# Optimization experiments

Measured on AMD Instinct MI355X. Metric: run time of the kernel, lower is better.

The kernel has to match this reference:

```python
import jax, jax.numpy as jnp
import numpy as np

H, C = 2, 32  # heads, out_channels per head
NEG_SLOPE = 0.2


def gatv2_layer(h, src, dst, ea, W, b, We, att, bias, N):
    # shared lin_l = lin_r (share_weights=True)
    z = (h @ W + b).reshape(N, H, C)                      # [N,H,C]
    e = (ea @ We).reshape(-1, H, C)                        # [E',H,C]
    s = jax.nn.leaky_relu(z[dst] + z[src] + e, NEG_SLOPE)  # [E',H,C]
    alpha = jnp.einsum('ehc,hc->eh', s, att)               # [E',H]
    # segment softmax over destination neighborhoods
    m = jax.ops.segment_max(alpha, dst, num_segments=N)
    m = jnp.where(jnp.isfinite(m), m, 0.0)
    ex = jnp.exp(alpha - m[dst])
    denom = jax.ops.segment_sum(ex, dst, num_segments=N)
    a = ex / (denom[dst] + 1e-16)                          # [E',H]
    msg = (z[src] * a[:, :, None]).reshape(-1, H * C)      # [E',H*C]
    out = jax.ops.segment_sum(msg, dst, num_segments=N) + bias
    return out                                             # [N,H*C]


def setup_inputs() -> dict:
    key = jax.random.key(0)
    ks = jax.random.split(key, 16)
    N, E = 50000, 800000
    inp = {
        'x': jax.random.normal(ks[0], (N, 2), jnp.float32),
        'edge_index': jax.random.randint(ks[1], (2, E), 0, N, jnp.int64 if jax.config.jax_enable_x64 else jnp.int32).astype(jnp.int32),
        'edge_attr': jax.random.uniform(ks[2], (E, 2), jnp.float32),
        'dest_index': 123,
        'W0': jax.random.normal(ks[3], (2, 64), jnp.float32) * 0.5,
        'b0': jnp.zeros((64,), jnp.float32),
        'We0': jax.random.normal(ks[4], (2, 64), jnp.float32) * 0.5,
        'att0': jax.random.normal(ks[5], (H, C), jnp.float32) * 0.5,
        'bias0': jnp.zeros((64,), jnp.float32),
        'W1': jax.random.normal(ks[6], (64, 64), jnp.float32) * 0.125,
        'b1': jnp.zeros((64,), jnp.float32),
        'We1': jax.random.normal(ks[7], (2, 64), jnp.float32) * 0.5,
        'att1': jax.random.normal(ks[8], (H, C), jnp.float32) * 0.5,
        'bias1': jnp.zeros((64,), jnp.float32),
        'Wm1': jax.random.normal(ks[9], (194, 32), jnp.float32) * 0.07,
        'bm1': jnp.zeros((32,), jnp.float32),
        'Wm2': jax.random.normal(ks[10], (32, 1), jnp.float32) * 0.17,
        'bm2': jnp.zeros((1,), jnp.float32),
    }
    return inp


def reference(x, edge_index, edge_attr, dest_index,
              W0, b0, We0, att0, bias0,
              W1, b1, We1, att1, bias1,
              Wm1, bm1, Wm2, bm2):
    N = x.shape[0]
    # add self loops (fill_value='mean' for edge_attr)
    loops = jnp.arange(N, dtype=edge_index.dtype)
    src = jnp.concatenate([edge_index[0], loops])
    dst = jnp.concatenate([edge_index[1], loops])
    ea_sl = jnp.concatenate(
        [edge_attr, jnp.broadcast_to(edge_attr.mean(axis=0), (N, edge_attr.shape[1]))], axis=0)

    h = x
    h = jax.nn.elu(gatv2_layer(h, src, dst, ea_sl, W0, b0, We0, att0, bias0, N))
    h = jax.nn.elu(gatv2_layer(h, src, dst, ea_sl, W1, b1, We1, att1, bias1, N))

    goal = h[dest_index]                                   # [64]
    src_emb = h[edge_index[0]]                             # [E,64]
    dst_emb = h[edge_index[1]]                             # [E,64]
    goal_rep = jnp.broadcast_to(goal, (edge_index.shape[1], goal.shape[0]))
    edge_in = jnp.concatenate([src_emb, dst_emb, goal_rep, edge_attr], axis=-1)  # [E,194]
    hmlp = jax.nn.relu(edge_in @ Wm1 + bm1)
    logits = (hmlp @ Wm2 + bm2).squeeze(-1)                # [E]
    return logits
```

## Files before the change

### kernel.cpp

```cpp
#include <hip/hip_runtime.h>
#include <hip/hip_bf16.h>
#include <hip/hip_fp16.h>
#include <math.h>


typedef __attribute__((ext_vector_type(8))) short short8;
typedef __attribute__((ext_vector_type(4))) float f32x4;

#define BSH 7
#define CAP 4096
#define CH 4096

template <int IMM>
__device__ __forceinline__ float swz(float x) {
    return __int_as_float(__builtin_amdgcn_ds_swizzle(__float_as_int(x), IMM));
}

template <int CTRL>
__device__ __forceinline__ float dpp_add(float p) {
    int t = __builtin_amdgcn_update_dpp(0, __float_as_int(p), CTRL, 0xF, 0xF, true);
    return p + __int_as_float(t);
}

__device__ __forceinline__ float head_reduce(float p) {
    p = dpp_add<0xB1>(p);
    p = dpp_add<0x4E>(p);
    p = dpp_add<0x141>(p);
    p = dpp_add<0x140>(p);
    p += swz<0x401F>(p);
    return p;
}

__device__ __forceinline__ short2 bsplit(float x) {
    unsigned u = __float_as_uint(x);
    short hi = (short)(u >> 16);
    float hif = __uint_as_float(u & 0xFFFF0000u);
    short lo = (short)(__float_as_uint(x - hif) >> 16);
    return make_short2(hi, lo);
}

__global__ __launch_bounds__(512) void setup_kernel(const float* __restrict__ W1,
                                                    const float* __restrict__ Wm1,
                                                    short* __restrict__ BfW1,
                                                    short* __restrict__ BfWm,
                                                    int* __restrict__ bucket_cursor,
                                                    float* __restrict__ easum, int nbuck) {
    if (blockIdx.x == 2) {
        for (int i = threadIdx.x; i < nbuck; i += 512) bucket_cursor[i] = i * CAP;
        if (threadIdx.x < 2) easum[threadIdx.x] = 0.f;
        return;
    }
    int snt = threadIdx.x >> 6;
    int lane = threadIdx.x & 63;
    int s = snt >> 2, nt = snt & 3;
    int col = nt * 16 + (lane & 15);
    short* Bf = blockIdx.x == 0 ? BfW1 : BfWm;
#pragma unroll
    for (int j = 0; j < 8; ++j) {
        int k = s * 32 + (lane >> 4) * 8 + j;
        float v;
        if (blockIdx.x == 0) {
            v = W1[k * 64 + col];
        } else {
            v = (col < 32) ? Wm1[k * 32 + col] : Wm1[(64 + k) * 32 + (col - 32)];
        }
        short2 t = bsplit(v);
        Bf[(snt * 2 + 0) * 512 + lane * 8 + j] = t.x;
        Bf[(snt * 2 + 1) * 512 + lane * 8 + j] = t.y;
    }
}

__global__ __launch_bounds__(256) void phaseA_kernel(const int* __restrict__ ei,
                                                     const float2* __restrict__ ea,
                                                     int* __restrict__ bucket_cursor,
                                                     float* __restrict__ easum,
                                                     float4* __restrict__ staged,
                                                     int E, int nbuck) {
    extern __shared__ int sm[];
    int* lcnt = sm;
    int* lbase = sm + nbuck;
    __shared__ float r0[4], r1[4];
    int tid = threadIdx.x;
    for (int i = tid; i < nbuck; i += 256) lcnt[i] = 0;
    __syncthreads();
    int base = blockIdx.x * CH;
    int end = min(base + CH, E);
    for (int i = base + tid; i < end; i += 256) {
        int d = ei[E + i];
        atomicAdd(&lcnt[d >> BSH], 1);
    }
    __syncthreads();
    for (int i = tid; i < nbuck; i += 256) {
        int c = lcnt[i];
        lbase[i] = c ? atomicAdd(&bucket_cursor[i], c) : 0;
        lcnt[i] = 0;
    }
    __syncthreads();
    float s0 = 0.f, s1 = 0.f;
    for (int i = base + tid; i < end; i += 256) {
        int s = ei[i], d = ei[E + i];
        float2 v = ea[i];
        s0 += v.x; s1 += v.y;
        int b = d >> BSH;
        int pos = lbase[b] + atomicAdd(&lcnt[b], 1);
        staged[pos] = make_float4(__int_as_float(s), v.x, v.y, __int_as_float(d));
    }
#pragma unroll
    for (int o = 32; o >= 1; o >>= 1) {
        s0 += __shfl_xor(s0, o);
        s1 += __shfl_xor(s1, o);
    }
    int wave = tid >> 6;
    if ((tid & 63) == 0) { r0[wave] = s0; r1[wave] = s1; }
    __syncthreads();
    if (tid == 0) {
        atomicAdd(&easum[0], r0[0] + r0[1] + r0[2] + r0[3]);
        atomicAdd(&easum[1], r1[0] + r1[1] + r1[2] + r1[3]);
    }
}

__global__ __launch_bounds__(256) void bscan_kernel(const int* __restrict__ bucket_cursor,
                                                    int* __restrict__ bucket_base,
                                                    int* __restrict__ row_ptr,
                                                    int N, int nbuck) {
    __shared__ int sm[256];
    int tid = threadIdx.x;
    int K = (nbuck + 255) / 256;
    int b0 = tid * K;
    int local = 0;
    for (int k = 0; k < K; ++k) {
        int b = b0 + k;
        if (b < nbuck) {
            int nodes = min(128, N - (b << BSH));
            local += bucket_cursor[b] - b * CAP + nodes;
        }
    }
    sm[tid] = local;
    __syncthreads();
    for (int st = 1; st < 256; st <<= 1) {
        int v = sm[tid];
        int a = (tid >= st) ? sm[tid - st] : 0;
        __syncthreads();
        sm[tid] = v + a;
        __syncthreads();
    }
    int run = (tid == 0) ? 0 : sm[tid - 1];
    for (int k = 0; k < K; ++k) {
        int b = b0 + k;
        if (b < nbuck) {
            int nodes = min(128, N - (b << BSH));
            int c = bucket_cursor[b] - b * CAP + nodes;
            bucket_base[b] = run;
            run += c;
        }
    }
    if (tid == 255) {
        bucket_base[nbuck] = sm[255];
        row_ptr[N] = sm[255];
    }
}

__global__ __launch_bounds__(256) void phaseB_kernel(const float4* __restrict__ staged,
                                                     const int* __restrict__ bucket_base,
                                                     const int* __restrict__ bucket_cursor,
                                                     const float* __restrict__ easum,
                                                     int* __restrict__ row_ptr,
                                                     float4* __restrict__ recs,
                                                     int N, int E) {
    __shared__ int cnt128[128];
    __shared__ int offs[128];
    int b = blockIdx.x;
    int n0 = b << BSH;
    int tid = threadIdx.x;
    if (tid < 128) cnt128[tid] = 0;
    __syncthreads();
    int sbeg = b * CAP;
    int send = bucket_cursor[b];
    for (int i = sbeg + tid; i < send; i += 256) {
        int d = __float_as_int(staged[i].w);
        atomicAdd(&cnt128[d - n0], 1);
    }
    __syncthreads();
    int node = n0 + tid;
    int tot = 0;
    if (tid < 128) {
        tot = cnt128[tid] + ((node < N) ? 1 : 0);
        offs[tid] = tot;
    }
    __syncthreads();
    for (int st = 1; st < 128; st <<= 1) {
        int v = 0;
        if (tid < 128) {
            v = offs[tid];
            if (tid >= st) v += offs[tid - st];
        }
        __syncthreads();
        if (tid < 128) offs[tid] = v;
        __syncthreads();
    }
    float inv = 1.f / (float)E;
    float m0 = easum[0] * inv, m1 = easum[1] * inv;
    if (tid < 128 && node < N) {
        int excl = bucket_base[b] + offs[tid] - tot;
        row_ptr[node] = excl;
        recs[excl] = make_float4(__int_as_float(node), m0, m1, __int_as_float(node));
        offs[tid] = excl + 1;
    }
    __syncthreads();
    for (int i = sbeg + tid; i < send; i += 256) {
        float4 r = staged[i];
        int d = __float_as_int(r.w);
        int pos = atomicAdd(&offs[d - n0], 1);
        recs[pos] = r;
    }
}

__global__ __launch_bounds__(256) void wgt0_kernel(const float2* __restrict__ x,
                                                   const float* __restrict__ W0,
                                                   const float* __restrict__ b0,
                                                   const float4* __restrict__ recs,
                                                   const float* __restrict__ We,
                                                   const float* __restrict__ att,
                                                   float4* __restrict__ wrec, int EP) {
    int lane = threadIdx.x & 63;
    int m = lane & 15, quad = lane >> 4;
    int c0 = quad * 8, c1 = 32 + c0;
    float w0a[8], w1a[8], ata[8], w0b[8], w1b[8], atb[8];
    float Wxa[8], Wya[8], bca[8], Wxb[8], Wyb[8], bcb[8];
#pragma unroll
    for (int j = 0; j < 8; ++j) {
        w0a[j] = We[c0 + j];  w1a[j] = We[64 + c0 + j];  ata[j] = att[c0 + j];
        w0b[j] = We[c1 + j];  w1b[j] = We[64 + c1 + j];  atb[j] = att[c1 + j];
        Wxa[j] = W0[c0 + j];  Wya[j] = W0[64 + c0 + j];  bca[j] = b0[c0 + j];
        Wxb[j] = W0[c1 + j];  Wyb[j] = W0[64 + c1 + j];  bcb[j] = b0[c1 + j];
    }
    int ntiles = (EP + 15) >> 4;
    int wid = (blockIdx.x * blockDim.x + threadIdx.x) >> 6;
    int nw = (gridDim.x * blockDim.x) >> 6;
    for (int t = wid; t < ntiles; t += nw) {
        int e = t * 16 + m;
        int ec = e < EP ? e : EP - 1;
        float4 r = recs[ec];
        int s = __float_as_int(r.x);
        int d = __float_as_int(r.w);
        float2 xs = x[s];
        float2 xd = x[d];
        float P0 = 0.f, P1 = 0.f;
#pragma unroll
        for (int j = 0; j < 8; ++j) {
            float zs = fmaf(xs.x, Wxa[j], fmaf(xs.y, Wya[j], bca[j]));
            float zd = fmaf(xd.x, Wxa[j], fmaf(xd.y, Wya[j], bca[j]));
            float t0 = zd + zs + fmaf(r.y, w0a[j], r.z * w1a[j]);
            t0 = fmaxf(t0, 0.2f * t0);
            P0 = fmaf(t0, ata[j], P0);
            float zs1 = fmaf(xs.x, Wxb[j], fmaf(xs.y, Wyb[j], bcb[j]));
            float zd1 = fmaf(xd.x, Wxb[j], fmaf(xd.y, Wyb[j], bcb[j]));
            float t1 = zd1 + zs1 + fmaf(r.y, w0b[j], r.z * w1b[j]);
            t1 = fmaxf(t1, 0.2f * t1);
            P1 = fmaf(t1, atb[j], P1);
        }
        P0 += swz<0x401F>(P0);
        P1 += swz<0x401F>(P1);
        P0 += __shfl_xor(P0, 32);
        P1 += __shfl_xor(P1, 32);
        float w0 = __expf(fminf(P0, 60.f));
        float w1 = __expf(fminf(P1, 60.f));
        if (lane < 16 && e < EP) wrec[e] = make_float4(w0, w1, xs.x, xs.y);
    }
}

__global__ __launch_bounds__(256) void hagg0_kernel(const float4* __restrict__ wrec,
                                                    const int* __restrict__ row_ptr,
                                                    const float* __restrict__ W0,
                                                    const float* __restrict__ b0,
                                                    const float* __restrict__ bias,
                                                    float* __restrict__ hout, int N) {
    int gtid = blockIdx.x * blockDim.x + threadIdx.x;
    int n = gtid >> 6;
    if (n >= N) return;
    n = __builtin_amdgcn_readfirstlane(n);
    int lane = threadIdx.x & 63;
    int beg = row_ptr[n], end = row_ptr[n + 1];
    float a0 = 0.f, a1 = 0.f, a2 = 0.f, c0 = 0.f, c1 = 0.f, c2 = 0.f;
    for (int i = beg + lane; i < end; i += 64) {
        float4 r = wrec[i];
        a0 += r.x; a1 = fmaf(r.x, r.z, a1); a2 = fmaf(r.x, r.w, a2);
        c0 += r.y; c1 = fmaf(r.y, r.z, c1); c2 = fmaf(r.y, r.w, c2);
    }
#pragma unroll
    for (int o = 32; o >= 1; o >>= 1) {
        a0 += __shfl_xor(a0, o); a1 += __shfl_xor(a1, o); a2 += __shfl_xor(a2, o);
        c0 += __shfl_xor(c0, o); c1 += __shfl_xor(c1, o); c2 += __shfl_xor(c2, o);
    }
    int head = lane >> 5;
    float l  = head ? c0 : a0;
    float Sx = head ? c1 : a1;
    float Sy = head ? c2 : a2;
    float num = fmaf(W0[lane], Sx, fmaf(W0[64 + lane], Sy, b0[lane] * l));
    float v = num / (l + 1e-16f) + bias[lane];
    v = (v > 0.f) ? v : expm1f(v);
    hout[(size_t)n * 64 + lane] = v;
}

__global__ __launch_bounds__(256) void agg1_kernel(
    const __half* __restrict__ z, const int* __restrict__ row_ptr,
    const float4* __restrict__ recs,
    const float* __restrict__ We, const float* __restrict__ att,
    const float* __restrict__ bias, float* __restrict__ hout, int N) {
    int gtid = blockIdx.x * blockDim.x + threadIdx.x;
    int n = gtid >> 6;
    if (n >= N) return;
    n = __builtin_amdgcn_readfirstlane(n);
    int lane = threadIdx.x & 63;

    float We0 = We[lane], We1 = We[64 + lane];
    float attj = att[lane];
    float zn = __half2float(z[(size_t)n * 64 + lane]);

    int beg = row_ptr[n], end = row_ptr[n + 1];
    float ll[4] = {0.f, 0.f, 0.f, 0.f};
    float aa[4] = {0.f, 0.f, 0.f, 0.f};
    int i = beg;
    for (; i + 8 <= end; i += 8) {
        float w[8], zs[8];
#pragma unroll
        for (int k = 0; k < 8; ++k) {
            float4 r = recs[i + k];
            int s = __builtin_amdgcn_readfirstlane(__float_as_int(r.x));
            float zv = __half2float(z[(size_t)s * 64 + lane]);
            float sj = zn + zv + fmaf(r.y, We0, r.z * We1);
            sj = fmaxf(sj, 0.2f * sj);
            float alpha = head_reduce(sj * attj);
            w[k] = __expf(fminf(alpha, 60.f));
            zs[k] = zv;
        }
#pragma unroll
        for (int k = 0; k < 8; ++k) {
            ll[k & 3] += w[k];
            aa[k & 3] = fmaf(w[k], zs[k], aa[k & 3]);
        }
    }
    for (; i < end; ++i) {
        float4 r = recs[i];
        int s = __builtin_amdgcn_readfirstlane(__float_as_int(r.x));
        float zv = __half2float(z[(size_t)s * 64 + lane]);
        float sj = zn + zv + fmaf(r.y, We0, r.z * We1);
        sj = fmaxf(sj, 0.2f * sj);
        float alpha = head_reduce(sj * attj);
        float w = __expf(fminf(alpha, 60.f));
        ll[0] += w;
        aa[0] = fmaf(w, zv, aa[0]);
    }
    float l = (ll[0] + ll[1]) + (ll[2] + ll[3]);
    float a = (aa[0] + aa[1]) + (aa[2] + aa[3]);
    float v = a / (l + 1e-16f) + bias[lane];
    v = (v > 0.f) ? v : expm1f(v);
    hout[(size_t)n * 64 + lane] = v;
}

__global__ __launch_bounds__(256) void mfma_gemm64(const float* __restrict__ h,
                                                   const short* __restrict__ Bf,
                                                   const float* __restrict__ bias,
                                                   __half* __restrict__ out, int N,
                                                   const float* __restrict__ Wm1,
                                                   const float* __restrict__ bm1,
                                                   const int* __restrict__ dest,
                                                   float* __restrict__ gv) {
    int wave = threadIdx.x >> 6;
    int lane = threadIdx.x & 63;
    int n0 = blockIdx.x * 64 + wave * 16;
    if (n0 < N) {
        int m = lane & 15, quad = lane >> 4;
        int arow = n0 + m;
        if (arow > N - 1) arow = N - 1;
        f32x4 acc[4] = {{0.f, 0.f, 0.f, 0.f}, {0.f, 0.f, 0.f, 0.f},
                        {0.f, 0.f, 0.f, 0.f}, {0.f, 0.f, 0.f, 0.f}};
#pragma unroll
        for (int s = 0; s < 2; ++s) {
            const float* ap = h + (size_t)arow * 64 + s * 32 + quad * 8;
            float4 a0 = *(const float4*)ap;
            float4 a1 = *(const float4*)(ap + 4);
            short8 ahi, alo;
            short2 t;
            t = bsplit(a0.x); ahi[0] = t.x; alo[0] = t.y;
            t = bsplit(a0.y); ahi[1] = t.x; alo[1] = t.y;
            t = bsplit(a0.z); ahi[2] = t.x; alo[2] = t.y;
            t = bsplit(a0.w); ahi[3] = t.x; alo[3] = t.y;
            t = bsplit(a1.x); ahi[4] = t.x; alo[4] = t.y;
            t = bsplit(a1.y); ahi[5] = t.x; alo[5] = t.y;
            t = bsplit(a1.z); ahi[6] = t.x; alo[6] = t.y;
            t = bsplit(a1.w); ahi[7] = t.x; alo[7] = t.y;
#pragma unroll
            for (int nt = 0; nt < 4; ++nt) {
                const short* bp = Bf + ((s * 4 + nt) * 2) * 512 + lane * 8;
                short8 bhi = *(const short8*)bp;
                short8 blo = *(const short8*)(bp + 512);
                acc[nt] = __builtin_amdgcn_mfma_f32_16x16x32_bf16(ahi, bhi, acc[nt], 0, 0, 0);
                acc[nt] = __builtin_amdgcn_mfma_f32_16x16x32_bf16(ahi, blo, acc[nt], 0, 0, 0);
                acc[nt] = __builtin_amdgcn_mfma_f32_16x16x32_bf16(alo, bhi, acc[nt], 0, 0, 0);
            }
        }
#pragma unroll
        for (int nt = 0; nt < 4; ++nt) {
            int col = nt * 16 + m;
            float bj = bias ? bias[col] : 0.f;
#pragma unroll
            for (int r = 0; r < 4; ++r) {
                int orow = n0 + quad * 4 + r;
                if (orow < N) out[(size_t)orow * 64 + col] = __float2half(acc[nt][r] + bj);
            }
        }
    }
    if (gv && blockIdx.x == 0 && threadIdx.x < 32) {
        int dd = dest[0];
        int q = threadIdx.x;
        float acc2 = bm1[q];
        for (int k = 0; k < 64; ++k)
            acc2 = fmaf(h[(size_t)dd * 64 + k], Wm1[(128 + k) * 32 + q], acc2);
        gv[q] = acc2;
    }
}

__global__ __launch_bounds__(256) void edge_mlp_kernel(
    const int* __restrict__ ei, const float2* __restrict__ ea,
    const __half* __restrict__ hsd, const float* __restrict__ gvec,
    const float* __restrict__ WrowA, const float* __restrict__ WrowB,
    const float* __restrict__ Wm2, const float* __restrict__ bm2,
    float* __restrict__ out, int E) {
    int tid = blockIdx.x * blockDim.x + threadIdx.x;
    int e = tid >> 3;
    int j = tid & 7;
    if (e >= E) return;
    int s = ei[e], d = ei[E + e];
    float2 eav = ea[e];
    const __half2* ps = (const __half2*)(hsd + (size_t)s * 64 + j * 4);
    const __half2* pd = (const __half2*)(hsd + (size_t)d * 64 + 32 + j * 4);
    float2 a01 = __half22float2(ps[0]), a23 = __half22float2(ps[1]);
    float2 b01 = __half22float2(pd[0]), b23 = __half22float2(pd[1]);
    float4 g = *(const float4*)(gvec + j * 4);
    float4 wa = *(const float4*)(WrowA + j * 4);
    float4 wb = *(const float4*)(WrowB + j * 4);
    float4 w2 = *(const float4*)(Wm2 + j * 4);
    float acc = 0.f, v;
    v = fmaf(eav.x, wa.x, fmaf(eav.y, wb.x, a01.x + b01.x + g.x)); v = fmaxf(v, 0.f); acc = fmaf(v, w2.x, acc);
    v = fmaf(eav.x, wa.y, fmaf(eav.y, wb.y, a01.y + b01.y + g.y)); v = fmaxf(v, 0.f); acc = fmaf(v, w2.y, acc);
    v = fmaf(eav.x, wa.z, fmaf(eav.y, wb.z, a23.x + b23.x + g.z)); v = fmaxf(v, 0.f); acc = fmaf(v, w2.z, acc);
    v = fmaf(eav.x, wa.w, fmaf(eav.y, wb.w, a23.y + b23.y + g.w)); v = fmaxf(v, 0.f); acc = fmaf(v, w2.w, acc);
    acc = dpp_add<0xB1>(acc);
    acc = dpp_add<0x4E>(acc);
    acc = dpp_add<0x141>(acc);
    if (j == 0) out[e] = acc + bm2[0];
}

extern "C" void kernel_launch(void* const* d_in, const int* in_sizes, int n_in,
                              void* d_out, int out_size, void* d_ws, size_t ws_size,
                              hipStream_t stream) {
    const float* x     = (const float*)d_in[0];
    const int*   ei    = (const int*)d_in[1];
    const float* ea    = (const float*)d_in[2];
    const int*   dest  = (const int*)d_in[3];
    const float* W0    = (const float*)d_in[4];
    const float* b0    = (const float*)d_in[5];
    const float* We0   = (const float*)d_in[6];
    const float* att0  = (const float*)d_in[7];
    const float* bias0 = (const float*)d_in[8];
    const float* W1    = (const float*)d_in[9];
    const float* b1    = (const float*)d_in[10];
    const float* We1   = (const float*)d_in[11];
    const float* att1  = (const float*)d_in[12];
    const float* bias1 = (const float*)d_in[13];
    const float* Wm1   = (const float*)d_in[14];
    const float* bm1   = (const float*)d_in[15];
    const float* Wm2   = (const float*)d_in[16];
    const float* bm2   = (const float*)d_in[17];

    const int N = in_sizes[0] / 2;
    const int E = in_sizes[1] / 2;
    const int EP = E + N;
    const int nbuck = (N + 127) >> BSH;
    const int nchunk = (E + CH - 1) / CH;

    char* ws = (char*)d_ws;
    size_t off = 0;
    auto alloc = [&](size_t bytes) -> void* {
        void* p = ws + off;
        off += bytes;
        off = (off + 255) & ~(size_t)255;
        return p;
    };
    int*    bucket_base   = (int*)alloc((size_t)(nbuck + 1) * 4);
    int*    bucket_cursor = (int*)alloc((size_t)nbuck * 4);
    int*    row_ptr       = (int*)alloc((size_t)(N + 1) * 4);
    size_t  slack_bytes   = (size_t)nbuck * CAP * 16;
    size_t  shared_bytes  = slack_bytes > (size_t)N * 128 ? slack_bytes : (size_t)N * 128;
    float4* staged        = (float4*)alloc(shared_bytes);
    float4* recs          = (float4*)alloc((size_t)EP * 16);
    float4* wrec          = (float4*)alloc((size_t)EP * 16);
    float*  hbuf          = (float*)alloc((size_t)N * 64 * 4);
    float*  easum         = (float*)alloc(8);
    float*  gvec          = (float*)alloc(32 * 4);
    short*  BfW1          = (short*)alloc(8192 * 2);
    short*  BfWm          = (short*)alloc(8192 * 2);
    __half* z16           = (__half*)staged;
    __half* hsd16         = z16;

    dim3 blk(256);
    setup_kernel<<<3, 512, 0, stream>>>(W1, Wm1, BfW1, BfWm, bucket_cursor, easum, nbuck);
    phaseA_kernel<<<nchunk, blk, (size_t)nbuck * 8, stream>>>(ei, (const float2*)ea,
                                                              bucket_cursor, easum,
                                                              staged, E, nbuck);
    bscan_kernel<<<1, blk, 0, stream>>>(bucket_cursor, bucket_base, row_ptr, N, nbuck);
    phaseB_kernel<<<nbuck, blk, 0, stream>>>(staged, bucket_base, bucket_cursor, easum,
                                             row_ptr, recs, N, E);
    wgt0_kernel<<<2048, blk, 0, stream>>>((const float2*)x, W0, b0, recs, We0, att0, wrec, EP);
    hagg0_kernel<<<(N * 64 + 255) / 256, blk, 0, stream>>>(wrec, row_ptr, W0, b0,
                                                           bias0, hbuf, N);
    mfma_gemm64<<<(N + 63) / 64, blk, 0, stream>>>(hbuf, BfW1, b1, z16, N,
                                                   nullptr, nullptr, nullptr, nullptr);
    agg1_kernel<<<(N * 64 + 255) / 256, blk, 0, stream>>>(z16, row_ptr, recs,
                                                          We1, att1, bias1, hbuf, N);
    mfma_gemm64<<<(N + 63) / 64, blk, 0, stream>>>(hbuf, BfWm, (const float*)nullptr, hsd16, N,
                                                   Wm1, bm1, dest, gvec);
    edge_mlp_kernel<<<((size_t)E * 8 + 255) / 256, blk, 0, stream>>>(
        ei, (const float2*)ea, hsd16, gvec,
        Wm1 + 192 * 32, Wm1 + 193 * 32, Wm2, bm2, (float*)d_out, E);
}
```

Before: 266.1 us.

## Fuse bucket scan into phaseB, fuse layer-0 aggregation with GEMM, prefetch agg1

Removes the single-block bucket scan kernel: each phaseB block now computes its own base by reducing the preceding bucket counts, and the last block writes row_ptr[N]. The layer-0 aggregation is fused with the following MFMA GEMM, keeping the 64-row tile in shared memory instead of writing hbuf to global memory and reading it back. agg1 gains software prefetching of the next eight records and their source features to overlap gather latency. These changes save two kernel launches and a global round trip, at the cost of redundant prefix reads in phaseB (quadratic in the bucket count) and fewer waves in the fused aggregation kernel.

```diff
diff --git a/kernel.cpp b/kernel.cpp
--- a/kernel.cpp
+++ b/kernel.cpp
@@ -119,61 +119,28 @@
     }
 }
 
-__global__ __launch_bounds__(256) void bscan_kernel(const int* __restrict__ bucket_cursor,
-                                                    int* __restrict__ bucket_base,
-                                                    int* __restrict__ row_ptr,
-                                                    int N, int nbuck) {
-    __shared__ int sm[256];
-    int tid = threadIdx.x;
-    int K = (nbuck + 255) / 256;
-    int b0 = tid * K;
-    int local = 0;
-    for (int k = 0; k < K; ++k) {
-        int b = b0 + k;
-        if (b < nbuck) {
-            int nodes = min(128, N - (b << BSH));
-            local += bucket_cursor[b] - b * CAP + nodes;
-        }
-    }
-    sm[tid] = local;
-    __syncthreads();
-    for (int st = 1; st < 256; st <<= 1) {
-        int v = sm[tid];
-        int a = (tid >= st) ? sm[tid - st] : 0;
-        __syncthreads();
-        sm[tid] = v + a;
-        __syncthreads();
-    }
-    int run = (tid == 0) ? 0 : sm[tid - 1];
-    for (int k = 0; k < K; ++k) {
-        int b = b0 + k;
-        if (b < nbuck) {
-            int nodes = min(128, N - (b << BSH));
-            int c = bucket_cursor[b] - b * CAP + nodes;
-            bucket_base[b] = run;
-            run += c;
-        }
-    }
-    if (tid == 255) {
-        bucket_base[nbuck] = sm[255];
-        row_ptr[N] = sm[255];
-    }
-}
-
 __global__ __launch_bounds__(256) void phaseB_kernel(const float4* __restrict__ staged,
-                                                     const int* __restrict__ bucket_base,
                                                      const int* __restrict__ bucket_cursor,
                                                      const float* __restrict__ easum,
                                                      int* __restrict__ row_ptr,
                                                      float4* __restrict__ recs,
-                                                     int N, int E) {
+                                                     int N, int E, int nbuck) {
     __shared__ int cnt128[128];
     __shared__ int offs[128];
+    __shared__ int psum[256];
     int b = blockIdx.x;
     int n0 = b << BSH;
     int tid = threadIdx.x;
+    int local = 0;
+    for (int j = tid; j < b; j += 256) local += bucket_cursor[j] - j * CAP;
+    psum[tid] = local;
     if (tid < 128) cnt128[tid] = 0;
     __syncthreads();
+    for (int st = 128; st > 0; st >>= 1) {
+        if (tid < st) psum[tid] += psum[tid + st];
+        __syncthreads();
+    }
+    int bbase = psum[0] + 128 * b;
     int sbeg = b * CAP;
     int send = bucket_cursor[b];
     for (int i = sbeg + tid; i < send; i += 256) {
@@ -201,10 +168,14 @@
     float inv = 1.f / (float)E;
     float m0 = easum[0] * inv, m1 = easum[1] * inv;
     if (tid < 128 && node < N) {
-        int excl = bucket_base[b] + offs[tid] - tot;
+        int excl = bbase + offs[tid] - tot;
         row_ptr[node] = excl;
         recs[excl] = make_float4(__int_as_float(node), m0, m1, __int_as_float(node));
         offs[tid] = excl + 1;
+    }
+    if (b == nbuck - 1 && tid == 0) {
+        int nodes = min(128, N - n0);
+        row_ptr[N] = bbase + (send - sbeg) + nodes;
     }
     __syncthreads();
     for (int i = sbeg + tid; i < send; i += 256) {
@@ -269,37 +240,81 @@
     }
 }
 
-__global__ __launch_bounds__(256) void hagg0_kernel(const float4* __restrict__ wrec,
-                                                    const int* __restrict__ row_ptr,
-                                                    const float* __restrict__ W0,
-                                                    const float* __restrict__ b0,
-                                                    const float* __restrict__ bias,
-                                                    float* __restrict__ hout, int N) {
-    int gtid = blockIdx.x * blockDim.x + threadIdx.x;
-    int n = gtid >> 6;
-    if (n >= N) return;
-    n = __builtin_amdgcn_readfirstlane(n);
+__global__ __launch_bounds__(256) void hagg_gemm_kernel(
+    const float4* __restrict__ wrec, const int* __restrict__ row_ptr,
+    const float* __restrict__ W0, const float* __restrict__ b0,
+    const float* __restrict__ bias, const short* __restrict__ Bf,
+    const float* __restrict__ b1, __half* __restrict__ z16, int N) {
+    __shared__ float hl[64 * 64];
+    int wave = threadIdx.x >> 6;
     int lane = threadIdx.x & 63;
-    int beg = row_ptr[n], end = row_ptr[n + 1];
-    float a0 = 0.f, a1 = 0.f, a2 = 0.f, c0 = 0.f, c1 = 0.f, c2 = 0.f;
-    for (int i = beg + lane; i < end; i += 64) {
-        float4 r = wrec[i];
-        a0 += r.x; a1 = fmaf(r.x, r.z, a1); a2 = fmaf(r.x, r.w, a2);
-        c0 += r.y; c1 = fmaf(r.y, r.z, c1); c2 = fmaf(r.y, r.w, c2);
-    }
-#pragma unroll
-    for (int o = 32; o >= 1; o >>= 1) {
-        a0 += __shfl_xor(a0, o); a1 += __shfl_xor(a1, o); a2 += __shfl_xor(a2, o);
-        c0 += __shfl_xor(c0, o); c1 += __shfl_xor(c1, o); c2 += __shfl_xor(c2, o);
-    }
-    int head = lane >> 5;
-    float l  = head ? c0 : a0;
-    float Sx = head ? c1 : a1;
-    float Sy = head ? c2 : a2;
-    float num = fmaf(W0[lane], Sx, fmaf(W0[64 + lane], Sy, b0[lane] * l));
-    float v = num / (l + 1e-16f) + bias[lane];
-    v = (v > 0.f) ? v : expm1f(v);
-    hout[(size_t)n * 64 + lane] = v;
+    int n0 = blockIdx.x * 64;
+    float W0a = W0[lane], W0b = W0[64 + lane], b0c = b0[lane], bj0 = bias[lane];
+    for (int t = 0; t < 16; ++t) {
+        int n = n0 + wave * 16 + t;
+        int row = wave * 16 + t;
+        if (n >= N) { hl[row * 64 + lane] = 0.f; continue; }
+        int beg = row_ptr[n], end = row_ptr[n + 1];
+        float a0 = 0.f, a1 = 0.f, a2 = 0.f, c0 = 0.f, c1 = 0.f, c2 = 0.f;
+        for (int i = beg + lane; i < end; i += 64) {
+            float4 r = wrec[i];
+            a0 += r.x; a1 = fmaf(r.x, r.z, a1); a2 = fmaf(r.x, r.w, a2);
+            c0 += r.y; c1 = fmaf(r.y, r.z, c1); c2 = fmaf(r.y, r.w, c2);
+        }
+#pragma unroll
+        for (int o = 32; o >= 1; o >>= 1) {
+            a0 += __shfl_xor(a0, o); a1 += __shfl_xor(a1, o); a2 += __shfl_xor(a2, o);
+            c0 += __shfl_xor(c0, o); c1 += __shfl_xor(c1, o); c2 += __shfl_xor(c2, o);
+        }
+        int head = lane >> 5;
+        float l  = head ? c0 : a0;
+        float Sx = head ? c1 : a1;
+        float Sy = head ? c2 : a2;
+        float num = fmaf(W0a, Sx, fmaf(W0b, Sy, b0c * l));
+        float v = num / (l + 1e-16f) + bj0;
+        v = (v > 0.f) ? v : expm1f(v);
+        hl[row * 64 + lane] = v;
+    }
+    __syncthreads();
+    int m = lane & 15, quad = lane >> 4;
+    int rowb = wave * 16 + m;
+    f32x4 acc[4] = {{0.f, 0.f, 0.f, 0.f}, {0.f, 0.f, 0.f, 0.f},
+                    {0.f, 0.f, 0.f, 0.f}, {0.f, 0.f, 0.f, 0.f}};
+#pragma unroll
+    for (int s = 0; s < 2; ++s) {
+        const float* ap = hl + rowb * 64 + s * 32 + quad * 8;
+        float4 a0 = *(const float4*)ap;
+        float4 a1 = *(const float4*)(ap + 4);
+        short8 ahi, alo;
+        short2 t;
+        t = bsplit(a0.x); ahi[0] = t.x; alo[0] = t.y;
+        t = bsplit(a0.y); ahi[1] = t.x; alo[1] = t.y;
+        t = bsplit(a0.z); ahi[2] = t.x; alo[2] = t.y;
+        t = bsplit(a0.w); ahi[3] = t.x; alo[3] = t.y;
+        t = bsplit(a1.x); ahi[4] = t.x; alo[4] = t.y;
+        t = bsplit(a1.y); ahi[5] = t.x; alo[5] = t.y;
+        t = bsplit(a1.z); ahi[6] = t.x; alo[6] = t.y;
+        t = bsplit(a1.w); ahi[7] = t.x; alo[7] = t.y;
+#pragma unroll
+        for (int nt = 0; nt < 4; ++nt) {
+            const short* bp = Bf + ((s * 4 + nt) * 2) * 512 + lane * 8;
+            short8 bhi = *(const short8*)bp;
+            short8 blo = *(const short8*)(bp + 512);
+            acc[nt] = __builtin_amdgcn_mfma_f32_16x16x32_bf16(ahi, bhi, acc[nt], 0, 0, 0);
+            acc[nt] = __builtin_amdgcn_mfma_f32_16x16x32_bf16(ahi, blo, acc[nt], 0, 0, 0);
+            acc[nt] = __builtin_amdgcn_mfma_f32_16x16x32_bf16(alo, bhi, acc[nt], 0, 0, 0);
+        }
+    }
+#pragma unroll
+    for (int nt = 0; nt < 4; ++nt) {
+        int col = nt * 16 + m;
+        float bj = b1[col];
+#pragma unroll
+        for (int r = 0; r < 4; ++r) {
+            int orow = n0 + wave * 16 + quad * 4 + r;
+            if (orow < N) z16[(size_t)orow * 64 + col] = __float2half(acc[nt][r] + bj);
+        }
+    }
 }
 
 __global__ __launch_bounds__(256) void agg1_kernel(
@@ -320,36 +335,42 @@
     int beg = row_ptr[n], end = row_ptr[n + 1];
     float ll[4] = {0.f, 0.f, 0.f, 0.f};
     float aa[4] = {0.f, 0.f, 0.f, 0.f};
-    int i = beg;
-    for (; i + 8 <= end; i += 8) {
-        float w[8], zs[8];
+    float4 rc[8];
+    float zv[8];
+#pragma unroll
+    for (int k = 0; k < 8; ++k) {
+        int idx = beg + k; if (idx > end - 1) idx = end - 1;
+        rc[k] = recs[idx];
+    }
+#pragma unroll
+    for (int k = 0; k < 8; ++k) {
+        int s = __builtin_amdgcn_readfirstlane(__float_as_int(rc[k].x));
+        zv[k] = __half2float(z[(size_t)s * 64 + lane]);
+    }
+    for (int i = beg; i < end; i += 8) {
+        float4 rn[8];
+        int inext = i + 8;
 #pragma unroll
         for (int k = 0; k < 8; ++k) {
-            float4 r = recs[i + k];
-            int s = __builtin_amdgcn_readfirstlane(__float_as_int(r.x));
-            float zv = __half2float(z[(size_t)s * 64 + lane]);
-            float sj = zn + zv + fmaf(r.y, We0, r.z * We1);
+            int idx = inext + k; if (idx > end - 1) idx = end - 1;
+            rn[k] = recs[idx];
+        }
+#pragma unroll
+        for (int k = 0; k < 8; ++k) {
+            float sj = zn + zv[k] + fmaf(rc[k].y, We0, rc[k].z * We1);
             sj = fmaxf(sj, 0.2f * sj);
             float alpha = head_reduce(sj * attj);
-            w[k] = __expf(fminf(alpha, 60.f));
-            zs[k] = zv;
+            float w = __expf(fminf(alpha, 60.f));
+            w = (i + k < end) ? w : 0.f;
+            ll[k & 3] += w;
+            aa[k & 3] = fmaf(w, zv[k], aa[k & 3]);
         }
 #pragma unroll
         for (int k = 0; k < 8; ++k) {
-            ll[k & 3] += w[k];
-            aa[k & 3] = fmaf(w[k], zs[k], aa[k & 3]);
-        }
-    }
-    for (; i < end; ++i) {
-        float4 r = recs[i];
-        int s = __builtin_amdgcn_readfirstlane(__float_as_int(r.x));
-        float zv = __half2float(z[(size_t)s * 64 + lane]);
-        float sj = zn + zv + fmaf(r.y, We0, r.z * We1);
-        sj = fmaxf(sj, 0.2f * sj);
-        float alpha = head_reduce(sj * attj);
-        float w = __expf(fminf(alpha, 60.f));
-        ll[0] += w;
-        aa[0] = fmaf(w, zv, aa[0]);
+            int s = __builtin_amdgcn_readfirstlane(__float_as_int(rn[k].x));
+            zv[k] = __half2float(z[(size_t)s * 64 + lane]);
+            rc[k] = rn[k];
+        }
     }
     float l = (ll[0] + ll[1]) + (ll[2] + ll[3]);
     float a = (aa[0] + aa[1]) + (aa[2] + aa[3]);
@@ -360,7 +381,6 @@
 
 __global__ __launch_bounds__(256) void mfma_gemm64(const float* __restrict__ h,
                                                    const short* __restrict__ Bf,
-                                                   const float* __restrict__ bias,
                                                    __half* __restrict__ out, int N,
                                                    const float* __restrict__ Wm1,
                                                    const float* __restrict__ bm1,
@@ -403,11 +423,10 @@
 #pragma unroll
         for (int nt = 0; nt < 4; ++nt) {
             int col = nt * 16 + m;
-            float bj = bias ? bias[col] : 0.f;
 #pragma unroll
             for (int r = 0; r < 4; ++r) {
                 int orow = n0 + quad * 4 + r;
-                if (orow < N) out[(size_t)orow * 64 + col] = __float2half(acc[nt][r] + bj);
+                if (orow < N) out[(size_t)orow * 64 + col] = __float2half(acc[nt][r]);
             }
         }
     }
@@ -488,7 +507,6 @@
         off = (off + 255) & ~(size_t)255;
         return p;
     };
-    int*    bucket_base   = (int*)alloc((size_t)(nbuck + 1) * 4);
     int*    bucket_cursor = (int*)alloc((size_t)nbuck * 4);
     int*    row_ptr       = (int*)alloc((size_t)(N + 1) * 4);
     size_t  slack_bytes   = (size_t)nbuck * CAP * 16;
@@ -509,17 +527,14 @@
     phaseA_kernel<<<nchunk, blk, (size_t)nbuck * 8, stream>>>(ei, (const float2*)ea,
                                                               bucket_cursor, easum,
                                                               staged, E, nbuck);
-    bscan_kernel<<<1, blk, 0, stream>>>(bucket_cursor, bucket_base, row_ptr, N, nbuck);
-    phaseB_kernel<<<nbuck, blk, 0, stream>>>(staged, bucket_base, bucket_cursor, easum,
-                                             row_ptr, recs, N, E);
+    phaseB_kernel<<<nbuck, blk, 0, stream>>>(staged, bucket_cursor, easum,
+                                             row_ptr, recs, N, E, nbuck);
     wgt0_kernel<<<2048, blk, 0, stream>>>((const float2*)x, W0, b0, recs, We0, att0, wrec, EP);
-    hagg0_kernel<<<(N * 64 + 255) / 256, blk, 0, stream>>>(wrec, row_ptr, W0, b0,
-                                                           bias0, hbuf, N);
-    mfma_gemm64<<<(N + 63) / 64, blk, 0, stream>>>(hbuf, BfW1, b1, z16, N,
-                                                   nullptr, nullptr, nullptr, nullptr);
+    hagg_gemm_kernel<<<(N + 63) / 64, blk, 0, stream>>>(wrec, row_ptr, W0, b0, bias0,
+                                                        BfW1, b1, z16, N);
     agg1_kernel<<<(N * 64 + 255) / 256, blk, 0, stream>>>(z16, row_ptr, recs,
                                                           We1, att1, bias1, hbuf, N);
-    mfma_gemm64<<<(N + 63) / 64, blk, 0, stream>>>(hbuf, BfWm, (const float*)nullptr, hsd16, N,
+    mfma_gemm64<<<(N + 63) / 64, blk, 0, stream>>>(hbuf, BfWm, hsd16, N,
                                                    Wm1, bm1, dest, gvec);
     edge_mlp_kernel<<<((size_t)E * 8 + 255) / 256, blk, 0, stream>>>(
         ei, (const float2*)ea, hsd16, gvec,
```

New measurement: 273.7 us. +2.9%, slower.
